# Kernel optimization log

Hardware: AMD Instinct MI355X
Metric: run time of the kernel (lower is better)

## Reference

```python
import jax, jax.numpy as jnp
import numpy as np

G, N, E, D, K = 32, 512, 8192, 256, 2048
LAMB_EDGE = 1.0
LAMB_NODE = 0.0
CODEBOOK_WEIGHT = 1000.0
ALPHA = 100.0


def setup_inputs() -> dict:
    key = jax.random.key(0)
    ks = jax.random.split(key, 12)
    s = 1.0 / np.sqrt(D)
    return {
        'feats': jax.random.normal(ks[0], (G, N, D), jnp.float32),
        'src': jax.random.randint(ks[1], (G, E), 0, N, jnp.int32),
        'dst': jax.random.randint(ks[2], (G, E), 0, N, jnp.int32),
        'W1': jax.random.normal(ks[3], (D, D), jnp.float32) * s,
        'b1': jnp.zeros((D,), jnp.float32),
        'W2': jax.random.normal(ks[4], (D, D), jnp.float32) * s,
        'b2': jnp.zeros((D,), jnp.float32),
        'ln_gamma': jnp.ones((D,), jnp.float32),
        'ln_beta': jnp.zeros((D,), jnp.float32),
        'dec1_W': jax.random.normal(ks[5], (D, D), jnp.float32) * s,
        'dec1_b': jnp.zeros((D,), jnp.float32),
        'dec2_W': jax.random.normal(ks[6], (D, D), jnp.float32) * s,
        'dec2_b': jnp.zeros((D,), jnp.float32),
        'codebook': jax.random.normal(ks[7], (K, D), jnp.float32),
    }


def _graph_conv(x, src, dst, W, b):
    # DGL GraphConv, norm='both': D_out^{-1/2} -> sum aggregate -> D_in^{-1/2} -> linear -> relu
    ones_e = jnp.ones(src.shape[0], x.dtype)
    deg_out = jnp.clip(jax.ops.segment_sum(ones_e, src, num_segments=N), 1.0)
    deg_in = jnp.clip(jax.ops.segment_sum(ones_e, dst, num_segments=N), 1.0)
    h = x * jax.lax.rsqrt(deg_out)[:, None]
    m = jax.ops.segment_sum(h[src], dst, num_segments=N)
    m = m * jax.lax.rsqrt(deg_in)[:, None]
    return jax.nn.relu(m @ W + b)


def _layernorm(x, gamma, beta):
    mu = jnp.mean(x, axis=-1, keepdims=True)
    var = jnp.mean(jnp.square(x - mu), axis=-1, keepdims=True)
    return (x - mu) * jax.lax.rsqrt(var + 1e-5) * gamma + beta


def _edge_loss(qe, src, dst):
    # qe: [N, D] decoded node embeddings for one graph
    logits = qe @ qe.T  # [N, N]
    adj = jnp.zeros((N, N), qe.dtype).at[src, dst].set(1.0)
    mask = jnp.triu(jnp.ones((N, N), bool), k=1)
    num_possible = N * N / 2.0
    num_edges = jnp.sum(jnp.where(mask, adj, 0.0))
    pos_weight = (num_possible - num_edges) / (num_edges + 1e-6)
    # BCEWithLogits with pos_weight, mean over strict upper triangle
    per = pos_weight * adj * jax.nn.softplus(-logits) + (1.0 - adj) * jax.nn.softplus(logits)
    return jnp.sum(jnp.where(mask, per, 0.0)) / (N * (N - 1) / 2.0)


def reference(feats, src, dst, W1, b1, W2, b2, ln_gamma, ln_beta,
              dec1_W, dec1_b, dec2_W, dec2_b, codebook):
    conv = jax.vmap(_graph_conv, in_axes=(0, 0, 0, None, None))
    h1 = conv(feats, src, dst, W1, b1)              # [G, N, D]
    h1 = _layernorm(h1, ln_gamma, ln_beta)           # dropout eval = identity
    h2 = conv(h1, src, dst, W2, b2)                  # [G, N, D]

    hf = h2.reshape(G * N, D)
    # cosine-sim VQ
    xn = hf * jax.lax.rsqrt(jnp.sum(hf * hf, -1, keepdims=True) + 1e-12)
    cn = codebook * jax.lax.rsqrt(jnp.sum(codebook * codebook, -1, keepdims=True) + 1e-12)
    dist = xn @ cn.T                                 # [G*N, K] cosine similarities
    idx = jnp.argmax(dist, axis=-1)
    q = codebook[idx]
    q_st = hf + jax.lax.stop_gradient(q - hf)        # straight-through
    vq_loss = CODEBOOK_WEIGHT * jnp.mean(jnp.square(q - jax.lax.stop_gradient(hf)))

    quantized_edge = (q_st @ dec1_W + dec1_b).reshape(G, N, D)
    quantized_node = q_st @ dec2_W + dec2_b

    edge_losses = jax.vmap(_edge_loss)(quantized_edge, src, dst)  # [G]
    edge_rec_loss = LAMB_EDGE * jnp.mean(edge_losses)
    feature_rec_loss = LAMB_NODE * jnp.mean(jnp.square(hf - quantized_node))
    loss = feature_rec_loss + edge_rec_loss * ALPHA + vq_loss
    return loss
```

## Files before the change

kernel.cpp:

```cpp
#include <hip/hip_runtime.h>
#include <math.h>

#define G 32
#define N 512
#define E 8192
#define D 256
#define KCB 2048
#define GN (G * N)

typedef __bf16 bf16x8 __attribute__((ext_vector_type(8)));
typedef float f32x4 __attribute__((ext_vector_type(4)));

static const size_t OFF_SPOS   = 0;
static const size_t OFF_SNEG   = OFF_SPOS + 256;
static const size_t OFF_BEST   = OFF_SNEG + 256;
static const size_t ZERO_BYTES = OFF_BEST + (size_t)GN * 8;
static const size_t OFF_NEDGE  = ZERO_BYTES;
static const size_t OFF_VQPART = OFF_NEDGE + 256;
static const size_t OFF_ROWOFF = OFF_VQPART + (size_t)GN * 4;
static const size_t OFF_RS_OUT = OFF_ROWOFF + (size_t)GN * 4;
static const size_t OFF_RS_IN  = OFF_RS_OUT + (size_t)GN * 4;
static const size_t OFF_DEG_IN = OFF_RS_IN + (size_t)GN * 4;
static const size_t OFF_CSR    = OFF_DEG_IN + (size_t)GN * 4;
static const size_t OFF_ADJ    = OFF_CSR + (size_t)G * E * 4;
static const size_t OFF_RNC    = OFF_ADJ + (size_t)G * N * N / 8;
static const size_t OFF_W1T    = OFF_RNC + (size_t)KCB * 4;
static const size_t OFF_W2T    = OFF_W1T + (size_t)D * D * 2;
static const size_t OFF_DWT    = OFF_W2T + (size_t)D * D * 2;
static const size_t OFF_CBB    = OFF_DWT + (size_t)D * D * 2;
static const size_t OFF_FEB    = OFF_CBB + (size_t)KCB * D * 2;
static const size_t OFF_AGGB   = OFF_FEB + (size_t)GN * D * 2;
static const size_t OFF_BF32   = OFF_AGGB + (size_t)GN * D * 2;
static const size_t OFF_BCB    = OFF_BF32 + (size_t)GN * D * 4;

__global__ void __launch_bounds__(512) k_setup(
    const int* __restrict__ src, const int* __restrict__ dst,
    unsigned* __restrict__ adj, int* __restrict__ nedge, int* __restrict__ row_off_g,
    float* __restrict__ rs_in_g, float* __restrict__ rs_out_g,
    int* __restrict__ deg_in_g, int* __restrict__ csr_src,
    const float* __restrict__ W1, const float* __restrict__ W2,
    const float* __restrict__ dW, __bf16* __restrict__ W1t,
    __bf16* __restrict__ W2t, __bf16* __restrict__ dWt,
    const float* __restrict__ cb, __bf16* __restrict__ cbb, float* __restrict__ rnc,
    const float* __restrict__ feats, unsigned* __restrict__ featsb2) {
  __shared__ __align__(16) char smem[41088];
  int b = blockIdx.x, t = threadIdx.x;
  if (b < 32) {
    int g = b;
    unsigned* s_adj = (unsigned*)smem;
    int* s_deg_in = (int*)(smem + 32768);
    int* s_deg_out = (int*)(smem + 34816);
    int(*s_buf)[N] = (int(*)[N])(smem + 36864);
    int* s_red = (int*)(smem + 40960);
    for (int i = t; i < N * N / 32; i += 512) s_adj[i] = 0;
    s_deg_in[t] = 0;
    s_deg_out[t] = 0;
    __syncthreads();
    const int* sg = src + g * E;
    const int* dg = dst + g * E;
    int se[E / 512], de[E / 512];
    int ecount = 0;
#pragma unroll
    for (int j = 0; j < E / 512; ++j) {
      int s = sg[t + j * 512], d = dg[t + j * 512];
      se[j] = s; de[j] = d;
      atomicAdd(&s_deg_out[s], 1);
      atomicAdd(&s_deg_in[d], 1);
      if (s < d) {
        int bit = s * N + d;
        unsigned m = 1u << (bit & 31);
        unsigned old = atomicOr(&s_adj[bit >> 5], m);
        if (!(old & m)) ++ecount;
      }
    }
    __syncthreads();
    for (int off = 32; off; off >>= 1) ecount += __shfl_down(ecount, off);
    if ((t & 63) == 0) s_red[t >> 6] = ecount;
    __syncthreads();
    if (t == 0) {
      int tot = 0;
      for (int i = 0; i < 8; ++i) tot += s_red[i];
      nedge[g] = tot;
    }
    unsigned* adjg = adj + (size_t)g * (N * N / 32);
    for (int i = t; i < N * N / 32; i += 512) adjg[i] = s_adj[i];
    int own = s_deg_in[t];
    s_buf[0][t] = own;
    __syncthreads();
    int cur = 0;
    for (int off = 1; off < N; off <<= 1) {
      int v = s_buf[cur][t];
      if (t >= off) v += s_buf[cur][t - off];
      s_buf[cur ^ 1][t] = v;
      __syncthreads();
      cur ^= 1;
    }
    int roff = s_buf[cur][t] - own;
    row_off_g[g * N + t] = roff;
    deg_in_g[g * N + t] = own;
    rs_in_g[g * N + t] = rsqrtf(fmaxf((float)own, 1.0f));
    rs_out_g[g * N + t] = rsqrtf(fmaxf((float)s_deg_out[t], 1.0f));
    __syncthreads();
    s_deg_in[t] = roff;
    __syncthreads();
    int* csrg = csr_src + g * E;
#pragma unroll
    for (int j = 0; j < E / 512; ++j) {
      int slot = atomicAdd(&s_deg_in[de[j]], 1);
      csrg[slot] = se[j];
    }
  } else if (b < 224) {
    float(*tile)[33] = (float(*)[33])smem;
    int z = (b - 32) / 64, tt = (b - 32) % 64;
    int bx = (tt & 7) * 32, by = (tt >> 3) * 32;
    const float* in = z == 0 ? W1 : (z == 1 ? W2 : dW);
    __bf16* out = z == 0 ? W1t : (z == 1 ? W2t : dWt);
    int tx = t & 31, ty = t >> 5;
#pragma unroll
    for (int r = 0; r < 32; r += 16) tile[ty + r][tx] = in[(by + ty + r) * D + bx + tx];
    __syncthreads();
#pragma unroll
    for (int r = 0; r < 32; r += 16)
      out[(size_t)(bx + ty + r) * D + by + tx] = (__bf16)tile[tx][ty + r];
  } else if (b < 1248) {
    float* w = (float*)smem;
    int row = (b - 224) * 2 + (t >> 8);
    int col = t & 255;
    float v = cb[(size_t)row * D + col];
    cbb[(size_t)row * D + col] = (__bf16)v;
    float s2 = v * v;
    for (int off = 32; off; off >>= 1) s2 += __shfl_down(s2, off);
    if ((t & 63) == 0) w[t >> 6] = s2;
    __syncthreads();
    if (t == 0) rnc[row] = rsqrtf(w[0] + w[1] + w[2] + w[3] + 1e-12f);
    if (t == 256) rnc[row] = rsqrtf(w[4] + w[5] + w[6] + w[7] + 1e-12f);
  } else {
    int i0 = (b - 1248) * 2048 + t;
#pragma unroll
    for (int q = 0; q < 4; ++q) {
      int i = i0 + q * 512;
      float2 v = ((const float2*)feats)[i];
      union { __bf16 h[2]; unsigned u; } o;
      o.h[0] = (__bf16)v.x;
      o.h[1] = (__bf16)v.y;
      featsb2[i] = o.u;
    }
  }
}

__global__ void __launch_bounds__(128) k_aggregate(
    const unsigned* __restrict__ x2, const int* __restrict__ csr_src,
    const int* __restrict__ row_off, const int* __restrict__ deg_in,
    const float* __restrict__ rs_in, const float* __restrict__ rs_out,
    unsigned* __restrict__ out2) {
  int b = blockIdx.x;
  int g = ((b & 7) << 2) | (b >> 12);
  int n = (b >> 3) & 511;
  int gn = (g << 9) | n;
  int t = threadIdx.x;
  int cnt = deg_in[gn];
  int base = g * E + row_off[gn];
  __shared__ int sidx[128];
  __shared__ float sw[128];
  float ax = 0.f, ay = 0.f;
  for (int c0 = 0; c0 < cnt; c0 += 128) {
    int m = min(128, cnt - c0);
    if (t < m) {
      int s = csr_src[base + c0 + t];
      sidx[t] = s;
      sw[t] = rs_out[(g << 9) | s];
    }
    __syncthreads();
    for (int j = 0; j < m; ++j) {
      int s = sidx[j];
      float w = sw[j];
      unsigned v = x2[((size_t)((g << 9) | s) << 7) + t];
      ax += __uint_as_float(v << 16) * w;
      ay += __uint_as_float(v & 0xffff0000u) * w;
    }
    __syncthreads();
  }
  float ri = rs_in[gn];
  union { __bf16 h[2]; unsigned u; } o;
  o.h[0] = (__bf16)(ax * ri);
  o.h[1] = (__bf16)(ay * ri);
  out2[((size_t)gn << 7) + t] = o.u;
}

__device__ __forceinline__ void gload_lds16(const __bf16* g, __bf16* s) {
  __builtin_amdgcn_global_load_lds((const __attribute__((address_space(1))) void*)g,
                                   (__attribute__((address_space(3))) void*)s, 16, 0, 0);
}

__device__ __forceinline__ void mfma_core(const __bf16* __restrict__ Abase,
                                          const __bf16* __restrict__ Bbase,
                                          __bf16* sA, __bf16* sB, f32x4 (&acc)[4][4],
                                          int tid) {
  int wave = tid >> 6, lane = tid & 63;
  int wr = (wave >> 1) * 64, wc = (wave & 1) * 64;
  int m = lane & 15, quad = lane >> 4;
  for (int k0 = 0; k0 < 256; k0 += 32) {
#pragma unroll
    for (int c2 = 0; c2 < 2; ++c2) {
      int c = wave * 2 + c2;
      int row = c * 16 + (lane >> 2);
      int col = (lane & 3) * 8;
      gload_lds16(Abase + (size_t)row * 256 + k0 + col, sA + c * 512);
      gload_lds16(Bbase + (size_t)row * 256 + k0 + col, sB + c * 512);
    }
    __syncthreads();
    bf16x8 af[4], bfr[4];
#pragma unroll
    for (int i = 0; i < 4; ++i) {
      af[i] = *(const bf16x8*)&sA[(wr + i * 16 + m) * 32 + quad * 8];
      bfr[i] = *(const bf16x8*)&sB[(wc + i * 16 + m) * 32 + quad * 8];
    }
#pragma unroll
    for (int i = 0; i < 4; ++i)
#pragma unroll
      for (int j = 0; j < 4; ++j)
        acc[i][j] = __builtin_amdgcn_mfma_f32_16x16x32_bf16(af[i], bfr[j], acc[i][j], 0, 0, 0);
    __syncthreads();
  }
}

template <bool RELU, bool SF32, bool SBF16>
__global__ void __launch_bounds__(256) k_gemm_bf16(
    const __bf16* __restrict__ A, const __bf16* __restrict__ Bt,
    const float* __restrict__ bias, float* __restrict__ C, __bf16* __restrict__ Cb) {
  __shared__ __align__(16) __bf16 sA[4096], sB[4096];
  f32x4 acc[4][4] = {};
  int tid = threadIdx.x;
  int row0 = blockIdx.x * 128, col0 = blockIdx.y * 128;
  mfma_core(A + (size_t)row0 * 256, Bt + (size_t)col0 * 256, sA, sB, acc, tid);
  int wave = tid >> 6, lane = tid & 63;
  int wr = (wave >> 1) * 64, wc = (wave & 1) * 64, quad = lane >> 4, n16 = lane & 15;
#pragma unroll
  for (int j = 0; j < 4; ++j) {
    int col = col0 + wc + j * 16 + n16;
    float bs = bias[col];
#pragma unroll
    for (int i = 0; i < 4; ++i)
#pragma unroll
      for (int r = 0; r < 4; ++r) {
        int row = row0 + wr + i * 16 + quad * 4 + r;
        float v = acc[i][j][r] + bs;
        if (RELU) v = fmaxf(v, 0.f);
        if (SF32) C[(size_t)row * 256 + col] = v;
        if (SBF16) Cb[(size_t)row * 256 + col] = (__bf16)v;
      }
  }
}

__global__ void __launch_bounds__(256) k_gemm_dec1(
    const __bf16* __restrict__ cbb, const unsigned long long* __restrict__ best,
    const __bf16* __restrict__ Bt, const float* __restrict__ bias,
    __bf16* __restrict__ Cb) {
  __shared__ __align__(16) __bf16 sA[4096], sB[4096];
  f32x4 acc[4][4] = {};
  int tid = threadIdx.x, wave = tid >> 6, lane = tid & 63;
  int row0 = blockIdx.x * 128, col0 = blockIdx.y * 128;
  int wr = (wave >> 1) * 64, wc = (wave & 1) * 64;
  int m = lane & 15, quad = lane >> 4;
  int c0 = wave * 2, c1 = wave * 2 + 1;
  int idx0 = (int)(0xFFFFFFFFu -
                   (unsigned)(best[row0 + c0 * 16 + (lane >> 2)] & 0xFFFFFFFFull));
  int idx1 = (int)(0xFFFFFFFFu -
                   (unsigned)(best[row0 + c1 * 16 + (lane >> 2)] & 0xFFFFFFFFull));
  const __bf16* Bbase = Bt + (size_t)col0 * 256;
  for (int k0 = 0; k0 < 256; k0 += 32) {
    int col = (lane & 3) * 8;
    gload_lds16(cbb + (size_t)idx0 * 256 + k0 + col, sA + c0 * 512);
    gload_lds16(cbb + (size_t)idx1 * 256 + k0 + col, sA + c1 * 512);
    gload_lds16(Bbase + (size_t)(c0 * 16 + (lane >> 2)) * 256 + k0 + col, sB + c0 * 512);
    gload_lds16(Bbase + (size_t)(c1 * 16 + (lane >> 2)) * 256 + k0 + col, sB + c1 * 512);
    __syncthreads();
    bf16x8 af[4], bfr[4];
#pragma unroll
    for (int i = 0; i < 4; ++i) {
      af[i] = *(const bf16x8*)&sA[(wr + i * 16 + m) * 32 + quad * 8];
      bfr[i] = *(const bf16x8*)&sB[(wc + i * 16 + m) * 32 + quad * 8];
    }
#pragma unroll
    for (int i = 0; i < 4; ++i)
#pragma unroll
      for (int j = 0; j < 4; ++j)
        acc[i][j] = __builtin_amdgcn_mfma_f32_16x16x32_bf16(af[i], bfr[j], acc[i][j], 0, 0, 0);
    __syncthreads();
  }
  int n16 = lane & 15;
#pragma unroll
  for (int j = 0; j < 4; ++j) {
    int col = col0 + wc + j * 16 + n16;
    float bs = bias[col];
#pragma unroll
    for (int i = 0; i < 4; ++i)
#pragma unroll
      for (int r = 0; r < 4; ++r) {
        int row = row0 + wr + i * 16 + quad * 4 + r;
        Cb[(size_t)row * 256 + col] = (__bf16)(acc[i][j][r] + bs);
      }
  }
}

__global__ void __launch_bounds__(128) k_layernorm(
    unsigned* __restrict__ xb2, const float* __restrict__ gamma,
    const float* __restrict__ beta) {
  int row = blockIdx.x, t = threadIdx.x;
  unsigned u = xb2[row * 128 + t];
  float vx = __uint_as_float(u << 16), vy = __uint_as_float(u & 0xffff0000u);
  float s = vx + vy, s2 = vx * vx + vy * vy;
  for (int off = 32; off; off >>= 1) {
    s += __shfl_down(s, off);
    s2 += __shfl_down(s2, off);
  }
  __shared__ float w1[2], w2[2];
  if ((t & 63) == 0) { w1[t >> 6] = s; w2[t >> 6] = s2; }
  __syncthreads();
  float mu = (w1[0] + w1[1]) * (1.f / D);
  float m2 = (w2[0] + w2[1]) * (1.f / D);
  float rstd = rsqrtf(m2 - mu * mu + 1e-5f);
  float2 gm = ((const float2*)gamma)[t];
  float2 bt = ((const float2*)beta)[t];
  union { __bf16 h[2]; unsigned u; } o;
  o.h[0] = (__bf16)((vx - mu) * rstd * gm.x + bt.x);
  o.h[1] = (__bf16)((vy - mu) * rstd * gm.y + bt.y);
  xb2[row * 128 + t] = o.u;
}

__global__ void __launch_bounds__(256) k_vq_bf16(
    const __bf16* __restrict__ A, const __bf16* __restrict__ CBt,
    const float* __restrict__ rnc, unsigned long long* __restrict__ best) {
  __shared__ __align__(16) __bf16 sA[4096], sB[4096];
  f32x4 acc[4][4] = {};
  int tid = threadIdx.x;
  int row0 = blockIdx.x * 128, col0 = blockIdx.y * 128;
  mfma_core(A + (size_t)row0 * 256, CBt + (size_t)col0 * 256, sA, sB, acc, tid);
  int wave = tid >> 6, lane = tid & 63;
  int wr = (wave >> 1) * 64, wc = (wave & 1) * 64, quad = lane >> 4, n16 = lane & 15;
#pragma unroll
  for (int i = 0; i < 4; ++i) {
    unsigned long long cand[4] = {0ull, 0ull, 0ull, 0ull};
#pragma unroll
    for (int j = 0; j < 4; ++j) {
      int col = col0 + wc + j * 16 + n16;
      float rc = rnc[col];
#pragma unroll
      for (int r = 0; r < 4; ++r) {
        float sim = acc[i][j][r] * rc;
        unsigned u = __float_as_uint(sim);
        u = ((int)u >= 0) ? (u | 0x80000000u) : ~u;
        unsigned long long c64 =
            ((unsigned long long)u << 32) | (0xFFFFFFFFu - (unsigned)col);
        cand[r] = cand[r] > c64 ? cand[r] : c64;
      }
    }
#pragma unroll
    for (int off = 1; off < 16; off <<= 1)
#pragma unroll
      for (int r = 0; r < 4; ++r) {
        unsigned long long o = __shfl_xor(cand[r], off, 64);
        cand[r] = cand[r] > o ? cand[r] : o;
      }
    if (n16 == 0)
#pragma unroll
      for (int r = 0; r < 4; ++r)
        atomicMax(&best[row0 + wr + i * 16 + quad * 4 + r], cand[r]);
  }
}

__global__ void k_vq_err(const unsigned long long* __restrict__ best,
                         const float* __restrict__ cb, const float* __restrict__ hf,
                         float* __restrict__ vq_part) {
  int row = blockIdx.x, t = threadIdx.x;
  unsigned long long b = best[row];
  int c = (int)(0xFFFFFFFFu - (unsigned)(b & 0xFFFFFFFFull));
  float d = cb[(size_t)c * D + t] - hf[(size_t)row * D + t];
  float s2 = d * d;
  for (int off = 32; off; off >>= 1) s2 += __shfl_down(s2, off);
  __shared__ float w[4];
  if ((t & 63) == 0) w[t >> 6] = s2;
  __syncthreads();
  if (t == 0) vq_part[row] = w[0] + w[1] + w[2] + w[3];
}

__constant__ int c_ti[10] = {0, 0, 0, 0, 1, 1, 1, 2, 2, 3};
__constant__ int c_tj[10] = {0, 1, 2, 3, 1, 2, 3, 2, 3, 3};

__global__ void __launch_bounds__(256) k_edge_bf16(
    const __bf16* __restrict__ qe, const unsigned* __restrict__ adj,
    float* __restrict__ Spos, float* __restrict__ Sneg) {
  int g = blockIdx.x / 10, p = blockIdx.x % 10;
  int row0 = c_ti[p] * 128, col0 = c_tj[p] * 128;
  const __bf16* Ag = qe + (size_t)g * N * D;
  const unsigned* adjg = adj + (size_t)g * (N * N / 32);
  __shared__ __align__(16) __bf16 sA[4096], sB[4096];
  f32x4 acc[4][4] = {};
  int tid = threadIdx.x;
  mfma_core(Ag + (size_t)row0 * 256, Ag + (size_t)col0 * 256, sA, sB, acc, tid);
  int wave = tid >> 6, lane = tid & 63;
  int wr = (wave >> 1) * 64, wc = (wave & 1) * 64, quad = lane >> 4, n16 = lane & 15;
  float spos = 0.f, sneg = 0.f;
#pragma unroll
  for (int i = 0; i < 4; ++i)
#pragma unroll
    for (int j = 0; j < 4; ++j) {
      int c = col0 + wc + j * 16 + n16;
#pragma unroll
      for (int r = 0; r < 4; ++r) {
        int rr = row0 + wr + i * 16 + quad * 4 + r;
        if (rr < c) {
          float l = acc[i][j][r];
          int bit = rr * N + c;
          bool a = (adjg[bit >> 5] >> (bit & 31)) & 1u;
          float spabs = log1pf(expf(-fabsf(l)));
          if (a) spos += fmaxf(-l, 0.f) + spabs;
          else sneg += fmaxf(l, 0.f) + spabs;
        }
      }
    }
  for (int off = 32; off; off >>= 1) {
    spos += __shfl_down(spos, off);
    sneg += __shfl_down(sneg, off);
  }
  __shared__ float wp[4], wn[4];
  if ((tid & 63) == 0) { wp[tid >> 6] = spos; wn[tid >> 6] = sneg; }
  __syncthreads();
  if (tid == 0) {
    atomicAdd(&Spos[g], wp[0] + wp[1] + wp[2] + wp[3]);
    atomicAdd(&Sneg[g], wn[0] + wn[1] + wn[2] + wn[3]);
  }
}

__global__ void __launch_bounds__(256) k_final(
    const int* __restrict__ nedge, const float* __restrict__ Spos,
    const float* __restrict__ Sneg, const float* __restrict__ vq_part,
    float* __restrict__ out) {
  int t = threadIdx.x;
  float vq = 0.f;
  for (int i = t; i < GN; i += 256) vq += vq_part[i];
  float el = 0.f;
  if (t < G) {
    float ne = (float)nedge[t];
    float pw = (131072.0f - ne) / (ne + 1e-6f);
    el = (pw * Spos[t] + Sneg[t]) * (1.0f / 130816.0f);
  }
  for (int off = 32; off; off >>= 1) {
    vq += __shfl_down(vq, off);
    el += __shfl_down(el, off);
  }
  __shared__ float wv[4], we[4];
  if ((t & 63) == 0) { wv[t >> 6] = vq; we[t >> 6] = el; }
  __syncthreads();
  if (t == 0) {
    float vqs = wv[0] + wv[1] + wv[2] + wv[3];
    float els = we[0] + we[1] + we[2] + we[3];
    out[0] = 100.0f * (els * (1.0f / G)) + 1000.0f * (vqs * (1.0f / ((float)GN * D)));
  }
}

extern "C" void kernel_launch(void* const* d_in, const int* in_sizes, int n_in,
                              void* d_out, int out_size, void* d_ws, size_t ws_size,
                              hipStream_t stream) {
  const float* feats = (const float*)d_in[0];
  const int* src = (const int*)d_in[1];
  const int* dst = (const int*)d_in[2];
  const float* W1 = (const float*)d_in[3];
  const float* b1 = (const float*)d_in[4];
  const float* W2 = (const float*)d_in[5];
  const float* b2 = (const float*)d_in[6];
  const float* ln_g = (const float*)d_in[7];
  const float* ln_b = (const float*)d_in[8];
  const float* dec1_W = (const float*)d_in[9];
  const float* dec1_b = (const float*)d_in[10];
  const float* cb = (const float*)d_in[13];

  char* ws = (char*)d_ws;
  float* Spos = (float*)(ws + OFF_SPOS);
  float* Sneg = (float*)(ws + OFF_SNEG);
  unsigned long long* best = (unsigned long long*)(ws + OFF_BEST);
  int* nedge = (int*)(ws + OFF_NEDGE);
  float* vq_part = (float*)(ws + OFF_VQPART);
  int* row_off = (int*)(ws + OFF_ROWOFF);
  float* rs_out = (float*)(ws + OFF_RS_OUT);
  float* rs_in = (float*)(ws + OFF_RS_IN);
  int* deg_in = (int*)(ws + OFF_DEG_IN);
  int* csr_src = (int*)(ws + OFF_CSR);
  unsigned* adj = (unsigned*)(ws + OFF_ADJ);
  float* rnc = (float*)(ws + OFF_RNC);
  __bf16* W1t = (__bf16*)(ws + OFF_W1T);
  __bf16* W2t = (__bf16*)(ws + OFF_W2T);
  __bf16* dWt = (__bf16*)(ws + OFF_DWT);
  __bf16* cbb = (__bf16*)(ws + OFF_CBB);
  unsigned* featsb2 = (unsigned*)(ws + OFF_FEB);
  __bf16* aggb = (__bf16*)(ws + OFF_AGGB);
  unsigned* aggb2 = (unsigned*)(ws + OFF_AGGB);
  float* bf32 = (float*)(ws + OFF_BF32);
  __bf16* bcb = (__bf16*)(ws + OFF_BCB);
  unsigned* bcb2 = (unsigned*)(ws + OFF_BCB);

  hipMemsetAsync(d_ws, 0, ZERO_BYTES, stream);

  k_setup<<<2272, 512, 0, stream>>>(src, dst, adj, nedge, row_off, rs_in, rs_out,
                                    deg_in, csr_src, W1, W2, dec1_W, W1t, W2t, dWt,
                                    cb, cbb, rnc, feats, featsb2);

  k_aggregate<<<GN, 128, 0, stream>>>(featsb2, csr_src, row_off, deg_in, rs_in, rs_out,
                                      aggb2);
  k_gemm_bf16<true, false, true><<<dim3(GN / 128, 2), 256, 0, stream>>>(
      aggb, W1t, b1, nullptr, bcb);
  k_layernorm<<<GN, 128, 0, stream>>>(bcb2, ln_g, ln_b);

  k_aggregate<<<GN, 128, 0, stream>>>(bcb2, csr_src, row_off, deg_in, rs_in, rs_out, aggb2);
  k_gemm_bf16<true, true, true><<<dim3(GN / 128, 2), 256, 0, stream>>>(
      aggb, W2t, b2, bf32, bcb);

  k_vq_bf16<<<dim3(GN / 128, KCB / 128), 256, 0, stream>>>(bcb, cbb, rnc, best);
  k_vq_err<<<GN, 256, 0, stream>>>(best, cb, bf32, vq_part);
  k_gemm_dec1<<<dim3(GN / 128, 2), 256, 0, stream>>>(cbb, best, dWt, dec1_b, aggb);
  k_edge_bf16<<<10 * G, 256, 0, stream>>>(aggb, adj, Spos, Sneg);

  k_final<<<1, 256, 0, stream>>>(nedge, Spos, Sneg, vq_part, (float*)d_out);
}
```

Measured before the change: 267.1 us.

## Keep VQ A-tile resident in LDS across codebook tiles; fuse vq_err into dec1

The VQ similarity kernel now loads the full 128x256 bf16 A block into LDS once and loops over four 128-column codebook tiles. It keeps per-row argmax candidates in registers across those tiles, which cuts A reloads and atomicMax traffic by a factor of four. The separate k_vq_err launch is removed and its per-row squared-error reduction moved into the blockIdx.y==0 blocks of k_gemm_dec1. In exchange, the VQ grid has a quarter as many blocks and uses 72KB of LDS, which lowers occupancy, and the fused error work makes half the dec1 blocks longer.

```diff
diff --git a/kernel.cpp b/kernel.cpp
--- a/kernel.cpp
+++ b/kernel.cpp
@@ -255,7 +255,8 @@
 __global__ void __launch_bounds__(256) k_gemm_dec1(
     const __bf16* __restrict__ cbb, const unsigned long long* __restrict__ best,
     const __bf16* __restrict__ Bt, const float* __restrict__ bias,
-    __bf16* __restrict__ Cb) {
+    __bf16* __restrict__ Cb, const float* __restrict__ cb,
+    const float* __restrict__ hf, float* __restrict__ vq_part) {
   __shared__ __align__(16) __bf16 sA[4096], sB[4096];
   f32x4 acc[4][4] = {};
   int tid = threadIdx.x, wave = tid >> 6, lane = tid & 63;
@@ -301,6 +302,21 @@
         Cb[(size_t)row * 256 + col] = (__bf16)(acc[i][j][r] + bs);
       }
   }
+  if (blockIdx.y == 0) {
+    for (int rr = wave * 32; rr < wave * 32 + 32; ++rr) {
+      int row = row0 + rr;
+      int ci = (int)(0xFFFFFFFFu - (unsigned)(best[row] & 0xFFFFFFFFull));
+      float s2 = 0.f;
+#pragma unroll
+      for (int q = 0; q < 4; ++q) {
+        int col = q * 64 + lane;
+        float d = cb[(size_t)ci * 256 + col] - hf[(size_t)row * 256 + col];
+        s2 += d * d;
+      }
+      for (int off = 32; off; off >>= 1) s2 += __shfl_down(s2, off);
+      if (lane == 0) vq_part[row] = s2;
+    }
+  }
 }
 
 __global__ void __launch_bounds__(128) k_layernorm(
@@ -331,57 +347,89 @@
 __global__ void __launch_bounds__(256) k_vq_bf16(
     const __bf16* __restrict__ A, const __bf16* __restrict__ CBt,
     const float* __restrict__ rnc, unsigned long long* __restrict__ best) {
-  __shared__ __align__(16) __bf16 sA[4096], sB[4096];
-  f32x4 acc[4][4] = {};
-  int tid = threadIdx.x;
-  int row0 = blockIdx.x * 128, col0 = blockIdx.y * 128;
-  mfma_core(A + (size_t)row0 * 256, CBt + (size_t)col0 * 256, sA, sB, acc, tid);
-  int wave = tid >> 6, lane = tid & 63;
-  int wr = (wave >> 1) * 64, wc = (wave & 1) * 64, quad = lane >> 4, n16 = lane & 15;
+  __shared__ __align__(16) __bf16 sA[32768];
+  __shared__ __align__(16) __bf16 sB[4096];
+  int tid = threadIdx.x, wave = tid >> 6, lane = tid & 63;
+  int row0 = blockIdx.x * 128, colbase = blockIdx.y * 512;
+  int wr = (wave >> 1) * 64, wc = (wave & 1) * 64;
+  int m = lane & 15, quad = lane >> 4, n16 = lane & 15;
+  const __bf16* Abase = A + (size_t)row0 * 256;
+  {
+    int rowl = lane >> 2, coll = (lane & 3) * 8;
+#pragma unroll
+    for (int kc = 0; kc < 8; ++kc)
+#pragma unroll
+      for (int c2 = 0; c2 < 2; ++c2) {
+        int c = wave * 2 + c2;
+        gload_lds16(Abase + (size_t)(c * 16 + rowl) * 256 + kc * 32 + coll,
+                    sA + kc * 4096 + c * 512);
+      }
+  }
+  __syncthreads();
+  unsigned long long cand[4][4];
+#pragma unroll
+  for (int i = 0; i < 4; ++i)
+#pragma unroll
+    for (int r = 0; r < 4; ++r) cand[i][r] = 0ull;
+  for (int jt = 0; jt < 4; ++jt) {
+    int col0 = colbase + jt * 128;
+    const __bf16* Bbase = CBt + (size_t)col0 * 256;
+    f32x4 acc[4][4] = {};
+    for (int k0 = 0; k0 < 256; k0 += 32) {
+#pragma unroll
+      for (int c2 = 0; c2 < 2; ++c2) {
+        int c = wave * 2 + c2;
+        int row = c * 16 + (lane >> 2);
+        int col = (lane & 3) * 8;
+        gload_lds16(Bbase + (size_t)row * 256 + k0 + col, sB + c * 512);
+      }
+      __syncthreads();
+      bf16x8 af[4], bfr[4];
+      int kc = k0 >> 5;
+#pragma unroll
+      for (int i = 0; i < 4; ++i) {
+        af[i] = *(const bf16x8*)&sA[kc * 4096 + (wr + i * 16 + m) * 32 + quad * 8];
+        bfr[i] = *(const bf16x8*)&sB[(wc + i * 16 + m) * 32 + quad * 8];
+      }
+#pragma unroll
+      for (int i = 0; i < 4; ++i)
+#pragma unroll
+        for (int j = 0; j < 4; ++j)
+          acc[i][j] =
+              __builtin_amdgcn_mfma_f32_16x16x32_bf16(af[i], bfr[j], acc[i][j], 0, 0, 0);
+      __syncthreads();
+    }
+#pragma unroll
+    for (int i = 0; i < 4; ++i)
+#pragma unroll
+      for (int j = 0; j < 4; ++j) {
+        int col = col0 + wc + j * 16 + n16;
+        float rc = rnc[col];
+#pragma unroll
+        for (int r = 0; r < 4; ++r) {
+          float sim = acc[i][j][r] * rc;
+          unsigned u = __float_as_uint(sim);
+          u = ((int)u >= 0) ? (u | 0x80000000u) : ~u;
+          unsigned long long c64 =
+              ((unsigned long long)u << 32) | (0xFFFFFFFFu - (unsigned)col);
+          cand[i][r] = cand[i][r] > c64 ? cand[i][r] : c64;
+        }
+      }
+  }
 #pragma unroll
   for (int i = 0; i < 4; ++i) {
-    unsigned long long cand[4] = {0ull, 0ull, 0ull, 0ull};
-#pragma unroll
-    for (int j = 0; j < 4; ++j) {
-      int col = col0 + wc + j * 16 + n16;
-      float rc = rnc[col];
+#pragma unroll
+    for (int off = 1; off < 16; off <<= 1)
 #pragma unroll
       for (int r = 0; r < 4; ++r) {
-        float sim = acc[i][j][r] * rc;
-        unsigned u = __float_as_uint(sim);
-        u = ((int)u >= 0) ? (u | 0x80000000u) : ~u;
-        unsigned long long c64 =
-            ((unsigned long long)u << 32) | (0xFFFFFFFFu - (unsigned)col);
-        cand[r] = cand[r] > c64 ? cand[r] : c64;
-      }
-    }
-#pragma unroll
-    for (int off = 1; off < 16; off <<= 1)
-#pragma unroll
-      for (int r = 0; r < 4; ++r) {
-        unsigned long long o = __shfl_xor(cand[r], off, 64);
-        cand[r] = cand[r] > o ? cand[r] : o;
+        unsigned long long o = __shfl_xor(cand[i][r], off, 64);
+        cand[i][r] = cand[i][r] > o ? cand[i][r] : o;
       }
     if (n16 == 0)
 #pragma unroll
       for (int r = 0; r < 4; ++r)
-        atomicMax(&best[row0 + wr + i * 16 + quad * 4 + r], cand[r]);
-  }
-}
-
-__global__ void k_vq_err(const unsigned long long* __restrict__ best,
-                         const float* __restrict__ cb, const float* __restrict__ hf,
-                         float* __restrict__ vq_part) {
-  int row = blockIdx.x, t = threadIdx.x;
-  unsigned long long b = best[row];
-  int c = (int)(0xFFFFFFFFu - (unsigned)(b & 0xFFFFFFFFull));
-  float d = cb[(size_t)c * D + t] - hf[(size_t)row * D + t];
-  float s2 = d * d;
-  for (int off = 32; off; off >>= 1) s2 += __shfl_down(s2, off);
-  __shared__ float w[4];
-  if ((t & 63) == 0) w[t >> 6] = s2;
-  __syncthreads();
-  if (t == 0) vq_part[row] = w[0] + w[1] + w[2] + w[3];
+        atomicMax(&best[row0 + wr + i * 16 + quad * 4 + r], cand[i][r]);
+  }
 }
 
 __constant__ int c_ti[10] = {0, 0, 0, 0, 1, 1, 1, 2, 2, 3};
@@ -515,9 +563,9 @@
   k_gemm_bf16<true, true, true><<<dim3(GN / 128, 2), 256, 0, stream>>>(
       aggb, W2t, b2, bf32, bcb);
 
-  k_vq_bf16<<<dim3(GN / 128, KCB / 128), 256, 0, stream>>>(bcb, cbb, rnc, best);
-  k_vq_err<<<GN, 256, 0, stream>>>(best, cb, bf32, vq_part);
-  k_gemm_dec1<<<dim3(GN / 128, 2), 256, 0, stream>>>(cbb, best, dWt, dec1_b, aggb);
+  k_vq_bf16<<<dim3(GN / 128, KCB / 512), 256, 0, stream>>>(bcb, cbb, rnc, best);
+  k_gemm_dec1<<<dim3(GN / 128, 2), 256, 0, stream>>>(cbb, best, dWt, dec1_b, aggb,
+                                                     cb, bf32, vq_part);
   k_edge_bf16<<<10 * G, 256, 0, stream>>>(aggb, adj, Spos, Sneg);
 
   k_final<<<1, 256, 0, stream>>>(nedge, Spos, Sneg, vq_part, (float*)d_out);
```

New measurement: 282.4 us. +5.7%, slower.
